# Kernel tuning notes

Measured on AMD Instinct MI355X. Metric: run time of the kernel, lower is better.

Reference implementation:

```python
import jax, jax.numpy as jnp
import numpy as np
from jax import lax

DIM = 512
D_STATE = 16
D_CONV = 4
EXPAND = 2
E = EXPAND * DIM  # expanded_dim


def setup_inputs() -> dict:
    key = jax.random.key(0)
    ks = jax.random.split(key, 8)
    B_, L = 4, 2048
    x = jax.random.normal(ks[0], (B_, L, DIM), dtype=jnp.float32)
    # parameters (xavier-ish scaled random; exact init values don't matter for math)
    W_in = jax.random.normal(ks[1], (2 * E, DIM), dtype=jnp.float32) * (1.0 / np.sqrt(DIM))
    W_conv = jax.random.normal(ks[2], (E, 1, D_CONV), dtype=jnp.float32) * 0.3
    A = jax.random.normal(ks[3], (E, D_STATE), dtype=jnp.float32) * 0.5
    Bp = jax.random.normal(ks[4], (E, D_STATE), dtype=jnp.float32) * (1.0 / np.sqrt(D_STATE))
    Cp = jax.random.normal(ks[5], (E, D_STATE), dtype=jnp.float32) * (1.0 / np.sqrt(D_STATE))
    Dp = jnp.zeros((E,), dtype=jnp.float32)
    W_out = jax.random.normal(ks[6], (DIM, E), dtype=jnp.float32) * (1.0 / np.sqrt(E))
    return {"x": x, "W_in": W_in, "W_conv": W_conv, "A": A, "Bp": Bp, "Cp": Cp, "Dp": Dp, "W_out": W_out}


def reference(x, W_in, W_conv, A, Bp, Cp, Dp, W_out):
    residual = x
    b, l, _ = x.shape
    xp = jnp.einsum('bld,ed->ble', x, W_in)        # [b,l,2E]
    xs, gate = jnp.split(xp, 2, axis=-1)
    xs = xs * jax.nn.sigmoid(gate)                 # [b,l,E]
    # causal depthwise conv1d: torch pads both sides by K-1 then slices [:, :, :l]
    xc = lax.conv_general_dilated(
        xs.transpose(0, 2, 1), W_conv,
        window_strides=(1,), padding=[(D_CONV - 1, 0)],
        feature_group_count=E,
        dimension_numbers=('NCH', 'OIH', 'NCH'))     # [b,E,l]
    u = jax.nn.silu(xc.transpose(0, 2, 1))          # [b,l,E]
    Aneg = -jnp.exp(A)                              # [E,N]
    delta = jax.nn.sigmoid(jnp.einsum('bld,dn->bln', u, Bp))  # [b,l,N]
    A_bar = jnp.exp(jnp.einsum('dn,bln->bldn', Aneg, delta))  # [b,l,E,N]
    Bx = jnp.einsum('bln,dn->bldn', delta, Bp) * u[..., None]  # B_bar * x_t

    def step(h, inp):
        A_t, Bx_t = inp
        h = A_t * h + Bx_t                          # [b,E,N]
        y_t = jnp.einsum('bdn,dn->bd', h, Cp)
        return h, y_t

    h0 = jnp.zeros((b, E, D_STATE), dtype=x.dtype)
    _, ys = lax.scan(step, h0, (A_bar.transpose(1, 0, 2, 3), Bx.transpose(1, 0, 2, 3)))
    y = ys.transpose(1, 0, 2)                       # [b,l,E]
    y = y + Dp * u
    out = jnp.einsum('ble,de->bld', y, W_out)
    return out + residual
```

## Files before the change

### kernel.cpp

```cpp
#include <hip/hip_runtime.h>

#define DIM   512
#define EE    1024
#define NS    16
#define BB    4
#define LL    2048
#define MM    (BB*LL)
#define NC    64
#define CL    32

typedef __bf16 bf16x8 __attribute__((ext_vector_type(8)));
typedef __bf16 bf16x4 __attribute__((ext_vector_type(4)));
typedef float  f32x4  __attribute__((ext_vector_type(4)));
typedef _Float16 f16x8 __attribute__((ext_vector_type(8)));

static __device__ __forceinline__ float sigmoidf_(float x) {
    return 1.0f / (1.0f + __expf(-x));
}

#define GLOAD(gp, lp) __builtin_amdgcn_global_load_lds( \
    (const __attribute__((address_space(1))) unsigned int*)(const void*)(gp), \
    (__attribute__((address_space(3))) unsigned int*)(void*)(lp), 16, 0, 0)

__global__ __launch_bounds__(256) void k_tobf(
    const float* __restrict__ x, const float* __restrict__ Win,
    const float* __restrict__ Wout, const float* __restrict__ Bp,
    __bf16* __restrict__ xbf, __bf16* __restrict__ winbf,
    __bf16* __restrict__ woutbf, __bf16* __restrict__ bpT)
{
    int g = blockIdx.x * 256 + threadIdx.x;
    const int nx4 = MM * DIM / 4;
    const int nw4 = 2 * EE * DIM / 4;
    const int no4 = DIM * EE / 4;
    if (g < nx4) {
        f32x4 v = ((const f32x4*)x)[g];
        bf16x4 o; for (int j = 0; j < 4; ++j) o[j] = (__bf16)v[j];
        ((bf16x4*)xbf)[g] = o;
    } else if (g < nx4 + nw4) {
        int i = g - nx4;
        f32x4 v = ((const f32x4*)Win)[i];
        bf16x4 o; for (int j = 0; j < 4; ++j) o[j] = (__bf16)v[j];
        ((bf16x4*)winbf)[i] = o;
    } else if (g < nx4 + nw4 + no4) {
        int i = g - nx4 - nw4;
        f32x4 v = ((const f32x4*)Wout)[i];
        bf16x4 o; for (int j = 0; j < 4; ++j) o[j] = (__bf16)v[j];
        ((bf16x4*)woutbf)[i] = o;
    } else {
        int i = g - nx4 - nw4 - no4;
        int e = i >> 4, n = i & 15;
        bpT[n * EE + e] = (__bf16)Bp[i];
    }
}

__global__ __launch_bounds__(256, 4) void k_gemm1(
    const __bf16* __restrict__ Abf,
    const __bf16* __restrict__ Wbf,
    __bf16* __restrict__ xs)
{
    __shared__ __bf16 sA[128 * 64];
    __shared__ __bf16 sB0[64 * 64];
    __shared__ __bf16 sB1[64 * 64];

    int bid = blockIdx.x;
    int swz = (bid & 7) * 128 + (bid >> 3);
    int bm = swz >> 4;
    int bn = swz & 15;

    int t = threadIdx.x;
    int lane = t & 63;
    int w = t >> 6;
    int wm = (w >> 1) * 64;
    int wn = (w & 1) * 32;
    int r15 = lane & 15;
    int kq = lane >> 4;

    const __bf16* Agb  = Abf + (bm * 128) * DIM;
    const __bf16* B0gb = Wbf + (bn * 64) * DIM;
    const __bf16* B1gb = Wbf + (1024 + bn * 64) * DIM;

    f32x4 accx[4][2] = {};
    f32x4 accg[4][2] = {};

    for (int kt = 0; kt < 8; ++kt) {
        #pragma unroll
        for (int i_ = 0; i_ < 4; ++i_) {
            int c_ = i_ * 256 + t;
            int row_ = c_ >> 3;
            int ss_ = (c_ & 7) ^ (row_ & 7);
            GLOAD(Agb + kt * 64 + row_ * DIM + ss_ * 8, sA + (i_ * 256 + w * 64) * 8);
        }
        #pragma unroll
        for (int i_ = 0; i_ < 2; ++i_) {
            int c_ = i_ * 256 + t;
            int row_ = c_ >> 3;
            int ss_ = (c_ & 7) ^ (row_ & 7);
            GLOAD(B0gb + kt * 64 + row_ * DIM + ss_ * 8, sB0 + (i_ * 256 + w * 64) * 8);
            GLOAD(B1gb + kt * 64 + row_ * DIM + ss_ * 8, sB1 + (i_ * 256 + w * 64) * 8);
        }
        __syncthreads();
        #pragma unroll
        for (int ks = 0; ks < 2; ++ks) {
            int kcs = ks * 4 + kq;
            bf16x8 a[4], b0[2], b1[2];
            #pragma unroll
            for (int m = 0; m < 4; ++m) {
                int r = wm + m * 16 + r15;
                a[m] = *(const bf16x8*)&sA[r * 64 + (kcs ^ (r & 7)) * 8];
            }
            #pragma unroll
            for (int n = 0; n < 2; ++n) {
                int r = wn + n * 16 + r15;
                b0[n] = *(const bf16x8*)&sB0[r * 64 + (kcs ^ (r & 7)) * 8];
                b1[n] = *(const bf16x8*)&sB1[r * 64 + (kcs ^ (r & 7)) * 8];
            }
            #pragma unroll
            for (int m = 0; m < 4; ++m)
                #pragma unroll
                for (int n = 0; n < 2; ++n) {
                    accx[m][n] = __builtin_amdgcn_mfma_f32_16x16x32_bf16(a[m], b0[n], accx[m][n], 0, 0, 0);
                    accg[m][n] = __builtin_amdgcn_mfma_f32_16x16x32_bf16(a[m], b1[n], accg[m][n], 0, 0, 0);
                }
        }
        __syncthreads();
    }

    #pragma unroll
    for (int m = 0; m < 4; ++m)
        #pragma unroll
        for (int n = 0; n < 2; ++n)
            #pragma unroll
            for (int r = 0; r < 4; ++r) {
                int row = bm * 128 + wm + m * 16 + (lane >> 4) * 4 + r;
                int col = bn * 64 + wn + n * 16 + r15;
                float xv = accx[m][n][r];
                float gv = accg[m][n][r];
                xs[row * EE + col] = (__bf16)(xv * sigmoidf_(gv));
            }
}

__global__ __launch_bounds__(256) void k_convdelta(
    const __bf16* __restrict__ xs, const float* __restrict__ Wc,
    const __bf16* __restrict__ bpT,
    __bf16* __restrict__ u, float* __restrict__ delta)
{
    __shared__ __bf16 uS[8][1032];
    __shared__ float red[4][256];
    int bid = blockIdx.x;
    int r0b = bid * 8;
    int t = threadIdx.x;
    int cg_ = t & 127, rh = t >> 7;
    int e8 = cg_ << 3;
    int rr0 = r0b + rh * 4;
    int l0 = rr0 & (LL - 1);

    f32x4 wj[8];
    #pragma unroll
    for (int j = 0; j < 8; ++j) wj[j] = *(const f32x4*)&Wc[(e8 + j) * 4];
    bf16x8 z = {};
    bf16x8 win[7];
    #pragma unroll
    for (int i = 0; i < 7; ++i) {
        win[i] = (l0 + i >= 3) ? *(const bf16x8*)&xs[(rr0 + i - 3) * EE + e8] : z;
    }
    #pragma unroll
    for (int i = 0; i < 4; ++i) {
        bf16x8 out;
        #pragma unroll
        for (int j = 0; j < 8; ++j) {
            float a = (float)win[i][j] * wj[j][0] + (float)win[i + 1][j] * wj[j][1]
                    + (float)win[i + 2][j] * wj[j][2] + (float)win[i + 3][j] * wj[j][3];
            out[j] = (__bf16)(a * sigmoidf_(a));
        }
        *(bf16x8*)&u[(rr0 + i) * EE + e8] = out;
        *(bf16x8*)&uS[rh * 4 + i][e8] = out;
    }
    __syncthreads();

    int lane = t & 63, w = t >> 6;
    int ar = lane & 15, kc = (lane >> 4) << 3;
    f32x4 acc = {};
    #pragma unroll
    for (int k0 = 0; k0 < 256; k0 += 32) {
        int k = w * 256 + k0 + kc;
        bf16x8 a = *(const bf16x8*)&uS[ar & 7][k];
        bf16x8 b = *(const bf16x8*)&bpT[ar * EE + k];
        acc = __builtin_amdgcn_mfma_f32_16x16x32_bf16(a, b, acc, 0, 0, 0);
    }
    *(f32x4*)&red[w][lane * 4] = acc;
    __syncthreads();
    if (t < 32) {
        #pragma unroll
        for (int r = 0; r < 4; ++r) {
            float s = red[0][t * 4 + r] + red[1][t * 4 + r]
                    + red[2][t * 4 + r] + red[3][t * 4 + r];
            int row = (t >> 4) * 4 + r;
            int col = t & 15;
            delta[(r0b + row) * NS + col] = sigmoidf_(s);
        }
    }
}

__global__ __launch_bounds__(256, 4) void k_scan1(
    const __bf16* __restrict__ u, const float* __restrict__ delta,
    const float* __restrict__ A, const float* __restrict__ Bp,
    const float* __restrict__ Cp, const float* __restrict__ Dp,
    _Float16* __restrict__ hbuf, float* __restrict__ Dsum,
    __bf16* __restrict__ yloc)
{
    __shared__ __bf16 uS[CL * 256];
    __shared__ __bf16 yS[CL * 256];
    __shared__ float dls[CL * NS];
    int bid = blockIdx.x;
    int et = bid & 3;
    int c  = (bid >> 2) & (NC - 1);
    int b  = bid >> 8;
    int t  = threadIdx.x;
    int lane = t & 63, w = t >> 6;
    int e0 = et * 256;
    int tok0 = b * LL + c * CL;
    int e  = e0 + t;

    if (w < 2)
        GLOAD(delta + tok0 * NS + w * 256 + lane * 4, dls + w * 256);
    #pragma unroll
    for (int i = 0; i < 4; ++i) {
        int chunk = i * 256 + t;
        GLOAD(u + (tok0 + (chunk >> 5)) * EE + e0 + (chunk & 31) * 8,
              uS + (i * 256 + w * 64) * 8);
    }

    float Ae[NS], Bpr[NS], Cr[NS];
    #pragma unroll
    for (int q = 0; q < 4; ++q) {
        f32x4 av = *(const f32x4*)&A[e * NS + q * 4];
        f32x4 bv = *(const f32x4*)&Bp[e * NS + q * 4];
        f32x4 cv = *(const f32x4*)&Cp[e * NS + q * 4];
        #pragma unroll
        for (int j = 0; j < 4; ++j) {
            Ae[q * 4 + j]  = -__expf(av[j]) * 1.44269504f;
            Bpr[q * 4 + j] = bv[j];
            Cr[q * 4 + j]  = cv[j];
        }
    }
    float Dv = Dp[e];
    __syncthreads();

    if (et == 0 && t < NS) {
        float s = 0.f;
        #pragma unroll
        for (int l = 0; l < CL; ++l) s += dls[l * NS + t];
        Dsum[(b * NC + c) * NS + t] = s;
    }

    float h[NS] = {};
    for (int l = 0; l < CL; ++l) {
        float uv = (float)uS[l * 256 + t];
        float yv = Dv * uv;
        const f32x4* dr = (const f32x4*)&dls[l * NS];
        f32x4 dv[4] = {dr[0], dr[1], dr[2], dr[3]};
        #pragma unroll
        for (int j = 0; j < NS; ++j) {
            float d  = dv[j >> 2][j & 3];
            float ab = __builtin_amdgcn_exp2f(Ae[j] * d);
            h[j] = ab * h[j] + (d * Bpr[j]) * uv;
            yv += h[j] * Cr[j];
        }
        yS[l * 256 + t] = (__bf16)yv;
    }
    int basep = ((b * NC + c) * EE + e) * NS;
    f16x8 h0, h1;
    #pragma unroll
    for (int j = 0; j < 8; ++j) { h0[j] = (_Float16)h[j]; h1[j] = (_Float16)h[8 + j]; }
    *(f16x8*)&hbuf[basep] = h0;
    *(f16x8*)&hbuf[basep + 8] = h1;

    __syncthreads();
    #pragma unroll
    for (int i = 0; i < 4; ++i) {
        int chunk = i * 256 + t;
        *(bf16x8*)&yloc[(tok0 + (chunk >> 5)) * EE + e0 + (chunk & 31) * 8]
            = *(const bf16x8*)&yS[chunk * 8];
    }
}

__global__ __launch_bounds__(256) void k_fix(
    const float* __restrict__ A, const float* __restrict__ Dsum,
    _Float16* __restrict__ hbuf)
{
    int g = blockIdx.x * 256 + threadIdx.x;
    int b = g >> 14;
    int r = g & 16383;
    int n = r & 15;
    float Ae = -__expf(A[r]) * 1.44269504f;
    float h = 0.f;
    for (int c = 0; c < NC; ++c) {
        int idx = (b * NC + c) * (EE * NS) + r;
        float hl = (float)hbuf[idx];
        float P  = __builtin_amdgcn_exp2f(Ae * Dsum[(b * NC + c) * NS + n]);
        hbuf[idx] = (_Float16)h;
        h = P * h + hl;
    }
}

__global__ __launch_bounds__(256, 4) void k_scan2(
    const float* __restrict__ delta, const float* __restrict__ A,
    const float* __restrict__ Cp, const _Float16* __restrict__ hin,
    __bf16* __restrict__ y)
{
    int bid = blockIdx.x;
    int et = bid & 3;
    int c  = (bid >> 2) & (NC - 1);
    int b  = bid >> 8;
    if (c == 0) return;
    __shared__ __bf16 yS[CL * 256];
    __shared__ float dls[CL * NS];
    int t  = threadIdx.x;
    int lane = t & 63, w = t >> 6;
    int e0 = et * 256;
    int tok0 = b * LL + c * CL;
    int e  = e0 + t;

    if (w < 2)
        GLOAD(delta + tok0 * NS + w * 256 + lane * 4, dls + w * 256);
    #pragma unroll
    for (int i = 0; i < 4; ++i) {
        int chunk = i * 256 + t;
        GLOAD(y + (tok0 + (chunk >> 5)) * EE + e0 + (chunk & 31) * 8,
              yS + (i * 256 + w * 64) * 8);
    }

    int basep = ((b * NC + c) * EE + e) * NS;
    f16x8 hv0 = *(const f16x8*)&hin[basep];
    f16x8 hv1 = *(const f16x8*)&hin[basep + 8];
    float Ae[NS], g_[NS];
    #pragma unroll
    for (int q = 0; q < 4; ++q) {
        f32x4 av = *(const f32x4*)&A[e * NS + q * 4];
        f32x4 cv = *(const f32x4*)&Cp[e * NS + q * 4];
        #pragma unroll
        for (int j = 0; j < 4; ++j) {
            int jj = q * 4 + j;
            Ae[jj] = -__expf(av[j]) * 1.44269504f;
            float hvv = (jj < 8) ? (float)hv0[jj & 7] : (float)hv1[jj & 7];
            g_[jj] = cv[j] * hvv;
        }
    }
    __syncthreads();

    float D[NS] = {};
    for (int l = 0; l < CL; ++l) {
        const f32x4* dr = (const f32x4*)&dls[l * NS];
        f32x4 dv[4] = {dr[0], dr[1], dr[2], dr[3]};
        float corr = 0.f;
        #pragma unroll
        for (int j = 0; j < NS; ++j) {
            D[j] += dv[j >> 2][j & 3];
            corr += g_[j] * __builtin_amdgcn_exp2f(Ae[j] * D[j]);
        }
        int idx = l * 256 + t;
        yS[idx] = (__bf16)((float)yS[idx] + corr);
    }

    __syncthreads();
    #pragma unroll
    for (int i = 0; i < 4; ++i) {
        int chunk = i * 256 + t;
        *(bf16x8*)&y[(tok0 + (chunk >> 5)) * EE + e0 + (chunk & 31) * 8]
            = *(const bf16x8*)&yS[chunk * 8];
    }
}

__global__ __launch_bounds__(256, 2) void k_gemm2(
    const __bf16* __restrict__ Ybf,
    const __bf16* __restrict__ Wobf,
    const __bf16* __restrict__ xres,
    float* __restrict__ out)
{
    __shared__ __bf16 sA[128 * 64];
    __shared__ __bf16 sB[64 * 64];

    int bid = blockIdx.x;
    int swz = (bid & 7) * 64 + (bid >> 3);
    int bm = swz >> 3;
    int bn = swz & 7;

    int t = threadIdx.x;
    int lane = t & 63;
    int w = t >> 6;
    int wm = (w >> 1) * 64;
    int wn = (w & 1) * 32;
    int r15 = lane & 15;
    int kq = lane >> 4;

    const __bf16* Agb = Ybf + (bm * 128) * EE;
    const __bf16* Bgb = Wobf + (bn * 64) * EE;

    f32x4 acc[4][2] = {};

    for (int kt = 0; kt < 16; ++kt) {
        #pragma unroll
        for (int i_ = 0; i_ < 4; ++i_) {
            int c_ = i_ * 256 + t;
            int row_ = c_ >> 3;
            int ss_ = (c_ & 7) ^ (row_ & 7);
            GLOAD(Agb + kt * 64 + row_ * EE + ss_ * 8, sA + (i_ * 256 + w * 64) * 8);
        }
        #pragma unroll
        for (int i_ = 0; i_ < 2; ++i_) {
            int c_ = i_ * 256 + t;
            int row_ = c_ >> 3;
            int ss_ = (c_ & 7) ^ (row_ & 7);
            GLOAD(Bgb + kt * 64 + row_ * EE + ss_ * 8, sB + (i_ * 256 + w * 64) * 8);
        }
        __syncthreads();
        #pragma unroll
        for (int ks = 0; ks < 2; ++ks) {
            int kcs = ks * 4 + kq;
            bf16x8 a[4], bfr[2];
            #pragma unroll
            for (int m = 0; m < 4; ++m) {
                int r = wm + m * 16 + r15;
                a[m] = *(const bf16x8*)&sA[r * 64 + (kcs ^ (r & 7)) * 8];
            }
            #pragma unroll
            for (int n = 0; n < 2; ++n) {
                int r = wn + n * 16 + r15;
                bfr[n] = *(const bf16x8*)&sB[r * 64 + (kcs ^ (r & 7)) * 8];
            }
            #pragma unroll
            for (int m = 0; m < 4; ++m)
                #pragma unroll
                for (int n = 0; n < 2; ++n)
                    acc[m][n] = __builtin_amdgcn_mfma_f32_16x16x32_bf16(a[m], bfr[n], acc[m][n], 0, 0, 0);
        }
        __syncthreads();
    }

    #pragma unroll
    for (int m = 0; m < 4; ++m)
        #pragma unroll
        for (int n = 0; n < 2; ++n)
            #pragma unroll
            for (int r = 0; r < 4; ++r) {
                int row = bm * 128 + wm + m * 16 + (lane >> 4) * 4 + r;
                int col = bn * 64 + wn + n * 16 + r15;
                out[row * DIM + col] = acc[m][n][r] + (float)xres[row * DIM + col];
            }
}

extern "C" void kernel_launch(void* const* d_in, const int* in_sizes, int n_in,
                              void* d_out, int out_size, void* d_ws, size_t ws_size,
                              hipStream_t stream) {
    const float* x    = (const float*)d_in[0];
    const float* Win  = (const float*)d_in[1];
    const float* Wc   = (const float*)d_in[2];
    const float* A    = (const float*)d_in[3];
    const float* Bp   = (const float*)d_in[4];
    const float* Cp   = (const float*)d_in[5];
    const float* Dp   = (const float*)d_in[6];
    const float* Wout = (const float*)d_in[7];

    char* ws = (char*)d_ws;
    __bf16* woutbf = (__bf16*)(ws + 0);
    __bf16* bpT    = (__bf16*)(ws + 1048576);
    float*  delta  = (float*)(ws + 1081344);
    float*  Dsum   = (float*)(ws + 1605632);
    __bf16* ubf    = (__bf16*)(ws + 1622016);
    __bf16* xbf    = (__bf16*)(ws + 18399232);
    __bf16* winbf  = (__bf16*)(ws + 26787840);
    __bf16* xsbf   = (__bf16*)(ws + 28884992);
    __bf16* yloc   = (__bf16*)(ws + 28884992);
    _Float16* hbuf = (_Float16*)(ws + 45662208);

    k_tobf     <<<5696, 256, 0, stream>>>(x, Win, Wout, Bp, xbf, winbf, woutbf, bpT);
    k_gemm1    <<<1024, 256, 0, stream>>>(xbf, winbf, xsbf);
    k_convdelta<<<1024, 256, 0, stream>>>(xsbf, Wc, bpT, ubf, delta);
    k_scan1    <<<1024, 256, 0, stream>>>(ubf, delta, A, Bp, Cp, Dp, hbuf, Dsum, yloc);
    k_fix      <<<256, 256, 0, stream>>>(A, Dsum, hbuf);
    k_scan2    <<<1024, 256, 0, stream>>>(delta, A, Cp, hbuf, yloc);
    k_gemm2    <<<512, 256, 0, stream>>>(yloc, woutbf, xbf, (float*)d_out);
}
```

Before: 139.4 us.

## Recompute conv/silu in scan kernels and rerun full scan in pass two

Instead of writing u to global memory and having scan1 emit local outputs that scan2 corrects, u is now recomputed from xs via the causal conv and SiLU inside both scan kernels, using a 3-token halo. Scan1 only produces chunk-final states. Scan2 reruns the full recurrence from the fixed-up initial state and writes y directly. This removes the u write/read and the yloc round trip, at the cost of doing the full 16-state recurrence twice and recomputing the conv.

```diff
diff --git a/kernel.cpp b/kernel.cpp
--- a/kernel.cpp
+++ b/kernel.cpp
@@ -142,7 +142,7 @@
 __global__ __launch_bounds__(256) void k_convdelta(
     const __bf16* __restrict__ xs, const float* __restrict__ Wc,
     const __bf16* __restrict__ bpT,
-    __bf16* __restrict__ u, float* __restrict__ delta)
+    float* __restrict__ delta)
 {
     __shared__ __bf16 uS[8][1032];
     __shared__ float red[4][256];
@@ -172,7 +172,6 @@
                     + (float)win[i + 2][j] * wj[j][2] + (float)win[i + 3][j] * wj[j][3];
             out[j] = (__bf16)(a * sigmoidf_(a));
         }
-        *(bf16x8*)&u[(rr0 + i) * EE + e8] = out;
         *(bf16x8*)&uS[rh * 4 + i][e8] = out;
     }
     __syncthreads();
@@ -201,15 +200,13 @@
     }
 }
 
-__global__ __launch_bounds__(256, 4) void k_scan1(
-    const __bf16* __restrict__ u, const float* __restrict__ delta,
+__global__ __launch_bounds__(256) void k_scan1(
+    const __bf16* __restrict__ xs, const float* __restrict__ delta,
     const float* __restrict__ A, const float* __restrict__ Bp,
-    const float* __restrict__ Cp, const float* __restrict__ Dp,
-    _Float16* __restrict__ hbuf, float* __restrict__ Dsum,
-    __bf16* __restrict__ yloc)
-{
-    __shared__ __bf16 uS[CL * 256];
-    __shared__ __bf16 yS[CL * 256];
+    const float* __restrict__ Wc,
+    _Float16* __restrict__ hbuf, float* __restrict__ Dsum)
+{
+    __shared__ __bf16 xsS[40 * 256];
     __shared__ float dls[CL * NS];
     int bid = blockIdx.x;
     int et = bid & 3;
@@ -219,31 +216,35 @@
     int lane = t & 63, w = t >> 6;
     int e0 = et * 256;
     int tok0 = b * LL + c * CL;
+    int tokS = tok0 - 3;
     int e  = e0 + t;
 
     if (w < 2)
         GLOAD(delta + tok0 * NS + w * 256 + lane * 4, dls + w * 256);
     #pragma unroll
-    for (int i = 0; i < 4; ++i) {
+    for (int i = 0; i < 5; ++i) {
         int chunk = i * 256 + t;
-        GLOAD(u + (tok0 + (chunk >> 5)) * EE + e0 + (chunk & 31) * 8,
-              uS + (i * 256 + w * 64) * 8);
-    }
-
-    float Ae[NS], Bpr[NS], Cr[NS];
+        GLOAD(xs + (tokS + (chunk >> 5)) * EE + e0 + (chunk & 31) * 8,
+              xsS + (i * 256 + w * 64) * 8);
+    }
+
+    float Ae[NS], Bpr[NS];
     #pragma unroll
     for (int q = 0; q < 4; ++q) {
         f32x4 av = *(const f32x4*)&A[e * NS + q * 4];
         f32x4 bv = *(const f32x4*)&Bp[e * NS + q * 4];
-        f32x4 cv = *(const f32x4*)&Cp[e * NS + q * 4];
         #pragma unroll
         for (int j = 0; j < 4; ++j) {
             Ae[q * 4 + j]  = -__expf(av[j]) * 1.44269504f;
             Bpr[q * 4 + j] = bv[j];
-            Cr[q * 4 + j]  = cv[j];
-        }
-    }
-    float Dv = Dp[e];
+        }
+    }
+    f32x4 wc = *(const f32x4*)&Wc[e * 4];
+    __syncthreads();
+    if (c == 0 && t < 96) {
+        int row = t >> 5, c8 = t & 31;
+        *(bf16x8*)&xsS[row * 256 + c8 * 8] = (bf16x8){};
+    }
     __syncthreads();
 
     if (et == 0 && t < NS) {
@@ -253,10 +254,15 @@
         Dsum[(b * NC + c) * NS + t] = s;
     }
 
+    float w0 = (float)xsS[0 * 256 + t];
+    float w1 = (float)xsS[1 * 256 + t];
+    float w2 = (float)xsS[2 * 256 + t];
     float h[NS] = {};
     for (int l = 0; l < CL; ++l) {
-        float uv = (float)uS[l * 256 + t];
-        float yv = Dv * uv;
+        float w3 = (float)xsS[(l + 3) * 256 + t];
+        float a  = w0 * wc[0] + w1 * wc[1] + w2 * wc[2] + w3 * wc[3];
+        float uv = a * sigmoidf_(a);
+        w0 = w1; w1 = w2; w2 = w3;
         const f32x4* dr = (const f32x4*)&dls[l * NS];
         f32x4 dv[4] = {dr[0], dr[1], dr[2], dr[3]};
         #pragma unroll
@@ -264,9 +270,7 @@
             float d  = dv[j >> 2][j & 3];
             float ab = __builtin_amdgcn_exp2f(Ae[j] * d);
             h[j] = ab * h[j] + (d * Bpr[j]) * uv;
-            yv += h[j] * Cr[j];
-        }
-        yS[l * 256 + t] = (__bf16)yv;
+        }
     }
     int basep = ((b * NC + c) * EE + e) * NS;
     f16x8 h0, h1;
@@ -274,14 +278,6 @@
     for (int j = 0; j < 8; ++j) { h0[j] = (_Float16)h[j]; h1[j] = (_Float16)h[8 + j]; }
     *(f16x8*)&hbuf[basep] = h0;
     *(f16x8*)&hbuf[basep + 8] = h1;
-
-    __syncthreads();
-    #pragma unroll
-    for (int i = 0; i < 4; ++i) {
-        int chunk = i * 256 + t;
-        *(bf16x8*)&yloc[(tok0 + (chunk >> 5)) * EE + e0 + (chunk & 31) * 8]
-            = *(const bf16x8*)&yS[chunk * 8];
-    }
 }
 
 __global__ __launch_bounds__(256) void k_fix(
@@ -303,63 +299,82 @@
     }
 }
 
-__global__ __launch_bounds__(256, 4) void k_scan2(
-    const float* __restrict__ delta, const float* __restrict__ A,
-    const float* __restrict__ Cp, const _Float16* __restrict__ hin,
+__global__ __launch_bounds__(256) void k_scan2(
+    const __bf16* __restrict__ xs, const float* __restrict__ delta,
+    const float* __restrict__ A, const float* __restrict__ Bp,
+    const float* __restrict__ Cp, const float* __restrict__ Dp,
+    const float* __restrict__ Wc, const _Float16* __restrict__ hin,
     __bf16* __restrict__ y)
 {
+    __shared__ __bf16 xsS[40 * 256];
+    __shared__ __bf16 yS[CL * 256];
+    __shared__ float dls[CL * NS];
     int bid = blockIdx.x;
     int et = bid & 3;
     int c  = (bid >> 2) & (NC - 1);
     int b  = bid >> 8;
-    if (c == 0) return;
-    __shared__ __bf16 yS[CL * 256];
-    __shared__ float dls[CL * NS];
     int t  = threadIdx.x;
     int lane = t & 63, w = t >> 6;
     int e0 = et * 256;
     int tok0 = b * LL + c * CL;
+    int tokS = tok0 - 3;
     int e  = e0 + t;
 
     if (w < 2)
         GLOAD(delta + tok0 * NS + w * 256 + lane * 4, dls + w * 256);
     #pragma unroll
-    for (int i = 0; i < 4; ++i) {
+    for (int i = 0; i < 5; ++i) {
         int chunk = i * 256 + t;
-        GLOAD(y + (tok0 + (chunk >> 5)) * EE + e0 + (chunk & 31) * 8,
-              yS + (i * 256 + w * 64) * 8);
+        GLOAD(xs + (tokS + (chunk >> 5)) * EE + e0 + (chunk & 31) * 8,
+              xsS + (i * 256 + w * 64) * 8);
     }
 
     int basep = ((b * NC + c) * EE + e) * NS;
     f16x8 hv0 = *(const f16x8*)&hin[basep];
     f16x8 hv1 = *(const f16x8*)&hin[basep + 8];
-    float Ae[NS], g_[NS];
+    float Ae[NS], Bpr[NS], Cr[NS], h[NS];
     #pragma unroll
     for (int q = 0; q < 4; ++q) {
         f32x4 av = *(const f32x4*)&A[e * NS + q * 4];
+        f32x4 bv = *(const f32x4*)&Bp[e * NS + q * 4];
         f32x4 cv = *(const f32x4*)&Cp[e * NS + q * 4];
         #pragma unroll
         for (int j = 0; j < 4; ++j) {
             int jj = q * 4 + j;
-            Ae[jj] = -__expf(av[j]) * 1.44269504f;
-            float hvv = (jj < 8) ? (float)hv0[jj & 7] : (float)hv1[jj & 7];
-            g_[jj] = cv[j] * hvv;
-        }
-    }
-    __syncthreads();
-
-    float D[NS] = {};
+            Ae[jj]  = -__expf(av[j]) * 1.44269504f;
+            Bpr[jj] = bv[j];
+            Cr[jj]  = cv[j];
+            h[jj]   = (jj < 8) ? (float)hv0[jj & 7] : (float)hv1[jj & 7];
+        }
+    }
+    float Dv = Dp[e];
+    f32x4 wc = *(const f32x4*)&Wc[e * 4];
+    __syncthreads();
+    if (c == 0 && t < 96) {
+        int row = t >> 5, c8 = t & 31;
+        *(bf16x8*)&xsS[row * 256 + c8 * 8] = (bf16x8){};
+    }
+    __syncthreads();
+
+    float w0 = (float)xsS[0 * 256 + t];
+    float w1 = (float)xsS[1 * 256 + t];
+    float w2 = (float)xsS[2 * 256 + t];
     for (int l = 0; l < CL; ++l) {
+        float w3 = (float)xsS[(l + 3) * 256 + t];
+        float a  = w0 * wc[0] + w1 * wc[1] + w2 * wc[2] + w3 * wc[3];
+        float uv = a * sigmoidf_(a);
+        w0 = w1; w1 = w2; w2 = w3;
         const f32x4* dr = (const f32x4*)&dls[l * NS];
         f32x4 dv[4] = {dr[0], dr[1], dr[2], dr[3]};
-        float corr = 0.f;
+        float yv = Dv * uv;
         #pragma unroll
         for (int j = 0; j < NS; ++j) {
-            D[j] += dv[j >> 2][j & 3];
-            corr += g_[j] * __builtin_amdgcn_exp2f(Ae[j] * D[j]);
-        }
-        int idx = l * 256 + t;
-        yS[idx] = (__bf16)((float)yS[idx] + corr);
+            float d  = dv[j >> 2][j & 3];
+            float ab = __builtin_amdgcn_exp2f(Ae[j] * d);
+            h[j] = ab * h[j] + (d * Bpr[j]) * uv;
+            yv += h[j] * Cr[j];
+        }
+        yS[l * 256 + t] = (__bf16)yv;
     }
 
     __syncthreads();
@@ -466,18 +481,17 @@
     __bf16* bpT    = (__bf16*)(ws + 1048576);
     float*  delta  = (float*)(ws + 1081344);
     float*  Dsum   = (float*)(ws + 1605632);
-    __bf16* ubf    = (__bf16*)(ws + 1622016);
+    __bf16* yloc   = (__bf16*)(ws + 1622016);
     __bf16* xbf    = (__bf16*)(ws + 18399232);
     __bf16* winbf  = (__bf16*)(ws + 26787840);
     __bf16* xsbf   = (__bf16*)(ws + 28884992);
-    __bf16* yloc   = (__bf16*)(ws + 28884992);
     _Float16* hbuf = (_Float16*)(ws + 45662208);
 
     k_tobf     <<<5696, 256, 0, stream>>>(x, Win, Wout, Bp, xbf, winbf, woutbf, bpT);
     k_gemm1    <<<1024, 256, 0, stream>>>(xbf, winbf, xsbf);
-    k_convdelta<<<1024, 256, 0, stream>>>(xsbf, Wc, bpT, ubf, delta);
-    k_scan1    <<<1024, 256, 0, stream>>>(ubf, delta, A, Bp, Cp, Dp, hbuf, Dsum, yloc);
+    k_convdelta<<<1024, 256, 0, stream>>>(xsbf, Wc, bpT, delta);
+    k_scan1    <<<1024, 256, 0, stream>>>(xsbf, delta, A, Bp, Wc, hbuf, Dsum);
     k_fix      <<<256, 256, 0, stream>>>(A, Dsum, hbuf);
-    k_scan2    <<<1024, 256, 0, stream>>>(delta, A, Cp, hbuf, yloc);
+    k_scan2    <<<1024, 256, 0, stream>>>(xsbf, delta, A, Bp, Cp, Dp, Wc, hbuf, yloc);
     k_gemm2    <<<512, 256, 0, stream>>>(yloc, woutbf, xbf, (float*)d_out);
 }
```

New measurement: 142.8 us. +2.4%, slower.

## Recompute full scan in second pass instead of writing and correcting local outputs

Applied to the files above, without the earlier changes.

The first scan pass now only computes chunk-final states and delta sums, without producing or storing per-token outputs. The second pass loads the fixed-up carry-in state and reruns the full recurrence to write the outputs once. This removes one round trip of the intermediate output buffer through global memory and the extra bf16 rounding. In exchange the recurrence is computed twice and the second pass now also processes chunk zero.

```diff
diff --git a/kernel.cpp b/kernel.cpp
--- a/kernel.cpp
+++ b/kernel.cpp
@@ -204,9 +204,93 @@
 __global__ __launch_bounds__(256, 4) void k_scan1(
     const __bf16* __restrict__ u, const float* __restrict__ delta,
     const float* __restrict__ A, const float* __restrict__ Bp,
+    _Float16* __restrict__ hbuf, float* __restrict__ Dsum)
+{
+    __shared__ __bf16 uS[CL * 256];
+    __shared__ float dls[CL * NS];
+    int bid = blockIdx.x;
+    int et = bid & 3;
+    int c  = (bid >> 2) & (NC - 1);
+    int b  = bid >> 8;
+    int t  = threadIdx.x;
+    int lane = t & 63, w = t >> 6;
+    int e0 = et * 256;
+    int tok0 = b * LL + c * CL;
+    int e  = e0 + t;
+
+    if (w < 2)
+        GLOAD(delta + tok0 * NS + w * 256 + lane * 4, dls + w * 256);
+    #pragma unroll
+    for (int i = 0; i < 4; ++i) {
+        int chunk = i * 256 + t;
+        GLOAD(u + (tok0 + (chunk >> 5)) * EE + e0 + (chunk & 31) * 8,
+              uS + (i * 256 + w * 64) * 8);
+    }
+
+    float Ae[NS], Bpr[NS];
+    #pragma unroll
+    for (int q = 0; q < 4; ++q) {
+        f32x4 av = *(const f32x4*)&A[e * NS + q * 4];
+        f32x4 bv = *(const f32x4*)&Bp[e * NS + q * 4];
+        #pragma unroll
+        for (int j = 0; j < 4; ++j) {
+            Ae[q * 4 + j]  = -__expf(av[j]) * 1.44269504f;
+            Bpr[q * 4 + j] = bv[j];
+        }
+    }
+    __syncthreads();
+
+    if (et == 0 && t < NS) {
+        float s = 0.f;
+        #pragma unroll
+        for (int l = 0; l < CL; ++l) s += dls[l * NS + t];
+        Dsum[(b * NC + c) * NS + t] = s;
+    }
+
+    float h[NS] = {};
+    for (int l = 0; l < CL; ++l) {
+        float uv = (float)uS[l * 256 + t];
+        const f32x4* dr = (const f32x4*)&dls[l * NS];
+        f32x4 dv[4] = {dr[0], dr[1], dr[2], dr[3]};
+        #pragma unroll
+        for (int j = 0; j < NS; ++j) {
+            float d  = dv[j >> 2][j & 3];
+            float ab = __builtin_amdgcn_exp2f(Ae[j] * d);
+            h[j] = ab * h[j] + (d * Bpr[j]) * uv;
+        }
+    }
+    int basep = ((b * NC + c) * EE + e) * NS;
+    f16x8 h0, h1;
+    #pragma unroll
+    for (int j = 0; j < 8; ++j) { h0[j] = (_Float16)h[j]; h1[j] = (_Float16)h[8 + j]; }
+    *(f16x8*)&hbuf[basep] = h0;
+    *(f16x8*)&hbuf[basep + 8] = h1;
+}
+
+__global__ __launch_bounds__(256) void k_fix(
+    const float* __restrict__ A, const float* __restrict__ Dsum,
+    _Float16* __restrict__ hbuf)
+{
+    int g = blockIdx.x * 256 + threadIdx.x;
+    int b = g >> 14;
+    int r = g & 16383;
+    int n = r & 15;
+    float Ae = -__expf(A[r]) * 1.44269504f;
+    float h = 0.f;
+    for (int c = 0; c < NC; ++c) {
+        int idx = (b * NC + c) * (EE * NS) + r;
+        float hl = (float)hbuf[idx];
+        float P  = __builtin_amdgcn_exp2f(Ae * Dsum[(b * NC + c) * NS + n]);
+        hbuf[idx] = (_Float16)h;
+        h = P * h + hl;
+    }
+}
+
+__global__ __launch_bounds__(256, 4) void k_scan2(
+    const __bf16* __restrict__ u, const float* __restrict__ delta,
+    const float* __restrict__ A, const float* __restrict__ Bp,
     const float* __restrict__ Cp, const float* __restrict__ Dp,
-    _Float16* __restrict__ hbuf, float* __restrict__ Dsum,
-    __bf16* __restrict__ yloc)
+    const _Float16* __restrict__ hin, __bf16* __restrict__ y)
 {
     __shared__ __bf16 uS[CL * 256];
     __shared__ __bf16 yS[CL * 256];
@@ -230,7 +314,10 @@
               uS + (i * 256 + w * 64) * 8);
     }
 
-    float Ae[NS], Bpr[NS], Cr[NS];
+    int basep = ((b * NC + c) * EE + e) * NS;
+    f16x8 hv0 = *(const f16x8*)&hin[basep];
+    f16x8 hv1 = *(const f16x8*)&hin[basep + 8];
+    float Ae[NS], Bpr[NS], Cr[NS], h[NS];
     #pragma unroll
     for (int q = 0; q < 4; ++q) {
         f32x4 av = *(const f32x4*)&A[e * NS + q * 4];
@@ -238,27 +325,21 @@
         f32x4 cv = *(const f32x4*)&Cp[e * NS + q * 4];
         #pragma unroll
         for (int j = 0; j < 4; ++j) {
-            Ae[q * 4 + j]  = -__expf(av[j]) * 1.44269504f;
-            Bpr[q * 4 + j] = bv[j];
-            Cr[q * 4 + j]  = cv[j];
+            int jj = q * 4 + j;
+            Ae[jj]  = -__expf(av[j]) * 1.44269504f;
+            Bpr[jj] = bv[j];
+            Cr[jj]  = cv[j];
+            h[jj]   = (jj < 8) ? (float)hv0[jj & 7] : (float)hv1[jj & 7];
         }
     }
     float Dv = Dp[e];
     __syncthreads();
 
-    if (et == 0 && t < NS) {
-        float s = 0.f;
-        #pragma unroll
-        for (int l = 0; l < CL; ++l) s += dls[l * NS + t];
-        Dsum[(b * NC + c) * NS + t] = s;
-    }
-
-    float h[NS] = {};
     for (int l = 0; l < CL; ++l) {
         float uv = (float)uS[l * 256 + t];
-        float yv = Dv * uv;
         const f32x4* dr = (const f32x4*)&dls[l * NS];
         f32x4 dv[4] = {dr[0], dr[1], dr[2], dr[3]};
+        float yv = Dv * uv;
         #pragma unroll
         for (int j = 0; j < NS; ++j) {
             float d  = dv[j >> 2][j & 3];
@@ -267,99 +348,6 @@
             yv += h[j] * Cr[j];
         }
         yS[l * 256 + t] = (__bf16)yv;
-    }
-    int basep = ((b * NC + c) * EE + e) * NS;
-    f16x8 h0, h1;
-    #pragma unroll
-    for (int j = 0; j < 8; ++j) { h0[j] = (_Float16)h[j]; h1[j] = (_Float16)h[8 + j]; }
-    *(f16x8*)&hbuf[basep] = h0;
-    *(f16x8*)&hbuf[basep + 8] = h1;
-
-    __syncthreads();
-    #pragma unroll
-    for (int i = 0; i < 4; ++i) {
-        int chunk = i * 256 + t;
-        *(bf16x8*)&yloc[(tok0 + (chunk >> 5)) * EE + e0 + (chunk & 31) * 8]
-            = *(const bf16x8*)&yS[chunk * 8];
-    }
-}
-
-__global__ __launch_bounds__(256) void k_fix(
-    const float* __restrict__ A, const float* __restrict__ Dsum,
-    _Float16* __restrict__ hbuf)
-{
-    int g = blockIdx.x * 256 + threadIdx.x;
-    int b = g >> 14;
-    int r = g & 16383;
-    int n = r & 15;
-    float Ae = -__expf(A[r]) * 1.44269504f;
-    float h = 0.f;
-    for (int c = 0; c < NC; ++c) {
-        int idx = (b * NC + c) * (EE * NS) + r;
-        float hl = (float)hbuf[idx];
-        float P  = __builtin_amdgcn_exp2f(Ae * Dsum[(b * NC + c) * NS + n]);
-        hbuf[idx] = (_Float16)h;
-        h = P * h + hl;
-    }
-}
-
-__global__ __launch_bounds__(256, 4) void k_scan2(
-    const float* __restrict__ delta, const float* __restrict__ A,
-    const float* __restrict__ Cp, const _Float16* __restrict__ hin,
-    __bf16* __restrict__ y)
-{
-    int bid = blockIdx.x;
-    int et = bid & 3;
-    int c  = (bid >> 2) & (NC - 1);
-    int b  = bid >> 8;
-    if (c == 0) return;
-    __shared__ __bf16 yS[CL * 256];
-    __shared__ float dls[CL * NS];
-    int t  = threadIdx.x;
-    int lane = t & 63, w = t >> 6;
-    int e0 = et * 256;
-    int tok0 = b * LL + c * CL;
-    int e  = e0 + t;
-
-    if (w < 2)
-        GLOAD(delta + tok0 * NS + w * 256 + lane * 4, dls + w * 256);
-    #pragma unroll
-    for (int i = 0; i < 4; ++i) {
-        int chunk = i * 256 + t;
-        GLOAD(y + (tok0 + (chunk >> 5)) * EE + e0 + (chunk & 31) * 8,
-              yS + (i * 256 + w * 64) * 8);
-    }
-
-    int basep = ((b * NC + c) * EE + e) * NS;
-    f16x8 hv0 = *(const f16x8*)&hin[basep];
-    f16x8 hv1 = *(const f16x8*)&hin[basep + 8];
-    float Ae[NS], g_[NS];
-    #pragma unroll
-    for (int q = 0; q < 4; ++q) {
-        f32x4 av = *(const f32x4*)&A[e * NS + q * 4];
-        f32x4 cv = *(const f32x4*)&Cp[e * NS + q * 4];
-        #pragma unroll
-        for (int j = 0; j < 4; ++j) {
-            int jj = q * 4 + j;
-            Ae[jj] = -__expf(av[j]) * 1.44269504f;
-            float hvv = (jj < 8) ? (float)hv0[jj & 7] : (float)hv1[jj & 7];
-            g_[jj] = cv[j] * hvv;
-        }
-    }
-    __syncthreads();
-
-    float D[NS] = {};
-    for (int l = 0; l < CL; ++l) {
-        const f32x4* dr = (const f32x4*)&dls[l * NS];
-        f32x4 dv[4] = {dr[0], dr[1], dr[2], dr[3]};
-        float corr = 0.f;
-        #pragma unroll
-        for (int j = 0; j < NS; ++j) {
-            D[j] += dv[j >> 2][j & 3];
-            corr += g_[j] * __builtin_amdgcn_exp2f(Ae[j] * D[j]);
-        }
-        int idx = l * 256 + t;
-        yS[idx] = (__bf16)((float)yS[idx] + corr);
     }
 
     __syncthreads();
@@ -476,8 +464,8 @@
     k_tobf     <<<5696, 256, 0, stream>>>(x, Win, Wout, Bp, xbf, winbf, woutbf, bpT);
     k_gemm1    <<<1024, 256, 0, stream>>>(xbf, winbf, xsbf);
     k_convdelta<<<1024, 256, 0, stream>>>(xsbf, Wc, bpT, ubf, delta);
-    k_scan1    <<<1024, 256, 0, stream>>>(ubf, delta, A, Bp, Cp, Dp, hbuf, Dsum, yloc);
+    k_scan1    <<<1024, 256, 0, stream>>>(ubf, delta, A, Bp, hbuf, Dsum);
     k_fix      <<<256, 256, 0, stream>>>(A, Dsum, hbuf);
-    k_scan2    <<<1024, 256, 0, stream>>>(delta, A, Cp, hbuf, yloc);
+    k_scan2    <<<1024, 256, 0, stream>>>(ubf, delta, A, Bp, Cp, Dp, hbuf, yloc);
     k_gemm2    <<<512, 256, 0, stream>>>(yloc, woutbf, xbf, (float*)d_out);
 }
```

Result: faster. 133.5 us (-4.2%).
